# Performance work log

Measured on AMD Instinct MI355X. Metric: run time of the kernel, lower is better.

## Reference

```python
import jax, jax.numpy as jnp
import numpy as np

DIM_HID = 65536
NKERS = 500  # fixed by nn.Linear(dim_hid, 500) in the original module


def setup_inputs() -> dict:
    key = jax.random.key(0)
    k1, k2, k3, k4, k5 = jax.random.split(key, 5)
    inp = jax.random.normal(k1, (DIM_HID,), dtype=jnp.float32)
    weight = jax.random.normal(k2, (NKERS, DIM_HID), dtype=jnp.float32) * (1.0 / np.sqrt(DIM_HID))
    bias = jax.random.normal(k3, (NKERS,), dtype=jnp.float32)
    # variable-width kernels, each kwidths[i] in [1, NKERS]
    kwidths = jax.random.randint(k4, (NKERS,), 1, NKERS + 1, dtype=jnp.int32)
    kernels = jax.random.normal(k5, (NKERS, NKERS), dtype=jnp.float32)
    return {"input": inp, "weight": weight, "bias": bias, "kernels": kernels, "kwidths": kwidths}


def reference(input, weight, bias, kernels, kwidths):
    # y = self.coefs(input): [NKERS]
    y = weight @ input + bias
    # The torch loop  z[:kwidths[i]] += y[i] * kernels[i]  is exactly a
    # weighted sum of zero-padded kernel rows: mask row i beyond kwidths[i].
    col = jnp.arange(NKERS, dtype=kwidths.dtype)
    mask = col[None, :] < kwidths[:, None]            # [NKERS, NKERS] bool
    padded = jnp.where(mask, kernels, 0.0)            # zero-padded kernel bank
    z = y @ padded                                    # [NKERS]
    return z
```

## Files before the change

kernel.cpp:

```cpp
#include <hip/hip_runtime.h>

#define DIM_HID 65536
#define NKERS   500
#define NQ      4
#define QCHUNK  (DIM_HID / NQ)

typedef float f4 __attribute__((ext_vector_type(4)));

__global__ __launch_bounds__(256) void gemv_part_kernel(
    const float* __restrict__ W,
    const float* __restrict__ x,
    float* __restrict__ ws)
{
    const int bid = blockIdx.x;
    const int row = bid >> 2;
    const int q   = bid & 3;
    const int t   = threadIdx.x;

    const f4* __restrict__ Wq =
        reinterpret_cast<const f4*>(W + (size_t)row * DIM_HID + q * QCHUNK);
    const f4* __restrict__ xq =
        reinterpret_cast<const f4*>(x + q * QCHUNK);

    float s = 0.0f;
#pragma unroll 4
    for (int k = 0; k < 16; ++k) {
        const int idx = t + k * 256;
        f4 w = __builtin_nontemporal_load(&Wq[idx]);
        f4 v = xq[idx];
        s = fmaf(w.x, v.x, s);
        s = fmaf(w.y, v.y, s);
        s = fmaf(w.z, v.z, s);
        s = fmaf(w.w, v.w, s);
    }

#pragma unroll
    for (int off = 32; off > 0; off >>= 1)
        s += __shfl_down(s, off, 64);

    __shared__ float wsum[4];
    const int wave = t >> 6;
    const int lane = t & 63;
    if (lane == 0) wsum[wave] = s;
    __syncthreads();

    if (t == 0)
        ws[bid] = (wsum[0] + wsum[1]) + (wsum[2] + wsum[3]);
}

__global__ __launch_bounds__(256) void expand_kernel(
    const float* __restrict__ ws,
    const float* __restrict__ bias,
    const float* __restrict__ kernels,
    const int* __restrict__ kw,
    float* __restrict__ z)
{
    const int j = blockIdx.x;
    const int t = threadIdx.x;
    const f4* __restrict__ wsv = reinterpret_cast<const f4*>(ws);

    float acc = 0.0f;
#pragma unroll
    for (int k = 0; k < 2; ++k) {
        const int i = t + k * 256;
        if (i < NKERS) {
            f4 p = wsv[i];
            const float yi = ((p.x + p.y) + (p.z + p.w)) + bias[i];
            const int   w  = kw[i];
            const float kv = kernels[i * NKERS + j];
            if (j < w) acc = fmaf(yi, kv, acc);
        }
    }

#pragma unroll
    for (int off = 32; off > 0; off >>= 1)
        acc += __shfl_down(acc, off, 64);

    __shared__ float wsum[4];
    const int wave = t >> 6;
    const int lane = t & 63;
    if (lane == 0) wsum[wave] = acc;
    __syncthreads();

    if (t == 0)
        z[j] = (wsum[0] + wsum[1]) + (wsum[2] + wsum[3]);
}

extern "C" void kernel_launch(void* const* d_in, const int* in_sizes, int n_in,
                              void* d_out, int out_size, void* d_ws, size_t ws_size,
                              hipStream_t stream)
{
    const float* input   = (const float*)d_in[0];
    const float* weight  = (const float*)d_in[1];
    const float* bias    = (const float*)d_in[2];
    const float* kernels = (const float*)d_in[3];
    const int*   kwidths = (const int*)d_in[4];
    float* z  = (float*)d_out;
    float* ws = (float*)d_ws;

    gemv_part_kernel<<<NKERS * NQ, 256, 0, stream>>>(weight, input, ws);
    expand_kernel<<<NKERS, 256, 0, stream>>>(ws, bias, kernels, kwidths, z);
}
```

Baseline: 29.76 us.

## Restructure expand stage into row-tiled partial sums plus reduction; drop nontemporal loads

The second stage, which assigned one block per output column and read a strided column of the kernel bank, is replaced by 32 blocks. Each block processes 16 kernel rows with coalesced row reads and writes partial column sums, and a third single-block kernel reduces them. This targets uncoalesced strided access and redundant recomputation of y in every block. It costs an extra kernel launch and a serial reduction over 32 partials. The GEMV weight load also switches from a nontemporal to a normal load.

```diff
diff --git a/kernel.cpp b/kernel.cpp
--- a/kernel.cpp
+++ b/kernel.cpp
@@ -4,6 +4,10 @@
 #define NKERS   500
 #define NQ      4
 #define QCHUNK  (DIM_HID / NQ)
+
+#define ITILE   16
+#define NIB     32
+#define JPAD    512
 
 typedef float f4 __attribute__((ext_vector_type(4)));
 
@@ -26,7 +30,7 @@
 #pragma unroll 4
     for (int k = 0; k < 16; ++k) {
         const int idx = t + k * 256;
-        f4 w = __builtin_nontemporal_load(&Wq[idx]);
+        f4 w = Wq[idx];
         f4 v = xq[idx];
         s = fmaf(w.x, v.x, s);
         s = fmaf(w.y, v.y, s);
@@ -48,42 +52,49 @@
         ws[bid] = (wsum[0] + wsum[1]) + (wsum[2] + wsum[3]);
 }
 
-__global__ __launch_bounds__(256) void expand_kernel(
+__global__ __launch_bounds__(256) void expand_part_kernel(
     const float* __restrict__ ws,
     const float* __restrict__ bias,
     const float* __restrict__ kernels,
     const int* __restrict__ kw,
+    float* __restrict__ partial)
+{
+    const int ib = blockIdx.x;
+    const int t  = threadIdx.x;
+    const int j0 = t;
+    const int j1 = t + 256;
+    const f4* __restrict__ wsv = reinterpret_cast<const f4*>(ws);
+
+    float a0 = 0.0f, a1 = 0.0f;
+#pragma unroll
+    for (int ii = 0; ii < ITILE; ++ii) {
+        const int i = ib * ITILE + ii;
+        if (i < NKERS) {
+            const f4  p  = wsv[i];
+            const float yi = ((p.x + p.y) + (p.z + p.w)) + bias[i];
+            const int   w  = kw[i];
+            const float* krow = kernels + i * NKERS;
+            const float k0 = krow[j0];
+            const float k1 = (j1 < NKERS) ? krow[j1] : 0.0f;
+            if (j0 < w) a0 = fmaf(yi, k0, a0);
+            if (j1 < w) a1 = fmaf(yi, k1, a1);
+        }
+    }
+    partial[ib * JPAD + j0] = a0;
+    partial[ib * JPAD + j1] = a1;
+}
+
+__global__ __launch_bounds__(512) void expand_reduce_kernel(
+    const float* __restrict__ partial,
     float* __restrict__ z)
 {
-    const int j = blockIdx.x;
-    const int t = threadIdx.x;
-    const f4* __restrict__ wsv = reinterpret_cast<const f4*>(ws);
-
-    float acc = 0.0f;
+    const int j = threadIdx.x;
+    if (j >= NKERS) return;
+    float s = 0.0f;
 #pragma unroll
-    for (int k = 0; k < 2; ++k) {
-        const int i = t + k * 256;
-        if (i < NKERS) {
-            f4 p = wsv[i];
-            const float yi = ((p.x + p.y) + (p.z + p.w)) + bias[i];
-            const int   w  = kw[i];
-            const float kv = kernels[i * NKERS + j];
-            if (j < w) acc = fmaf(yi, kv, acc);
-        }
-    }
-
-#pragma unroll
-    for (int off = 32; off > 0; off >>= 1)
-        acc += __shfl_down(acc, off, 64);
-
-    __shared__ float wsum[4];
-    const int wave = t >> 6;
-    const int lane = t & 63;
-    if (lane == 0) wsum[wave] = acc;
-    __syncthreads();
-
-    if (t == 0)
-        z[j] = (wsum[0] + wsum[1]) + (wsum[2] + wsum[3]);
+    for (int ib = 0; ib < NIB; ++ib)
+        s += partial[ib * JPAD + j];
+    z[j] = s;
 }
 
 extern "C" void kernel_launch(void* const* d_in, const int* in_sizes, int n_in,
@@ -97,7 +108,9 @@
     const int*   kwidths = (const int*)d_in[4];
     float* z  = (float*)d_out;
     float* ws = (float*)d_ws;
+    float* pz = ws + 4096;
 
     gemv_part_kernel<<<NKERS * NQ, 256, 0, stream>>>(weight, input, ws);
-    expand_kernel<<<NKERS, 256, 0, stream>>>(ws, bias, kernels, kwidths, z);
+    expand_part_kernel<<<NIB, 256, 0, stream>>>(ws, bias, kernels, kwidths, pz);
+    expand_reduce_kernel<<<1, 512, 0, stream>>>(pz, z);
 }
```

Result: slower. 32.95 us (+10.7%).

## Process four weight rows per GEMV block over sixteen column chunks

Applied to the files above, without the earlier changes.

Each GEMV block now computes partial dot products for four rows over a 4096-element column chunk, so one x load is reused across four weight rows. The grid still has 2000 blocks, and each thread issues four independent wide loads per iteration, which gives more memory parallelism. Sixteen partials per row are written to the workspace and summed in the expand kernel. This adds register pressure and a larger reduction in the second kernel.

```diff
diff --git a/kernel.cpp b/kernel.cpp
--- a/kernel.cpp
+++ b/kernel.cpp
@@ -2,50 +2,70 @@
 
 #define DIM_HID 65536
 #define NKERS   500
-#define NQ      4
-#define QCHUNK  (DIM_HID / NQ)
+#define ROWS_PB 4
+#define NCHUNK  16
+#define CHUNK   (DIM_HID / NCHUNK)
 
 typedef float f4 __attribute__((ext_vector_type(4)));
 
-__global__ __launch_bounds__(256) void gemv_part_kernel(
+__global__ __launch_bounds__(256, 8) void gemv_part_kernel(
     const float* __restrict__ W,
     const float* __restrict__ x,
     float* __restrict__ ws)
 {
     const int bid = blockIdx.x;
-    const int row = bid >> 2;
-    const int q   = bid & 3;
+    const int rg  = bid >> 4;
+    const int q   = bid & 15;
+    const int r0  = rg * ROWS_PB;
     const int t   = threadIdx.x;
 
-    const f4* __restrict__ Wq =
-        reinterpret_cast<const f4*>(W + (size_t)row * DIM_HID + q * QCHUNK);
-    const f4* __restrict__ xq =
-        reinterpret_cast<const f4*>(x + q * QCHUNK);
+    const size_t base = (size_t)r0 * DIM_HID + (size_t)q * CHUNK;
+    const f4* __restrict__ W0 = reinterpret_cast<const f4*>(W + base);
+    const f4* __restrict__ W1 = reinterpret_cast<const f4*>(W + base + DIM_HID);
+    const f4* __restrict__ W2 = reinterpret_cast<const f4*>(W + base + 2 * DIM_HID);
+    const f4* __restrict__ W3 = reinterpret_cast<const f4*>(W + base + 3 * DIM_HID);
+    const f4* __restrict__ xq = reinterpret_cast<const f4*>(x + q * CHUNK);
 
-    float s = 0.0f;
-#pragma unroll 4
-    for (int k = 0; k < 16; ++k) {
+    float s0 = 0.0f, s1 = 0.0f, s2 = 0.0f, s3 = 0.0f;
+#pragma unroll 2
+    for (int k = 0; k < 4; ++k) {
         const int idx = t + k * 256;
-        f4 w = __builtin_nontemporal_load(&Wq[idx]);
-        f4 v = xq[idx];
-        s = fmaf(w.x, v.x, s);
-        s = fmaf(w.y, v.y, s);
-        s = fmaf(w.z, v.z, s);
-        s = fmaf(w.w, v.w, s);
+        const f4 v  = xq[idx];
+        const f4 w0 = __builtin_nontemporal_load(&W0[idx]);
+        const f4 w1 = __builtin_nontemporal_load(&W1[idx]);
+        const f4 w2 = __builtin_nontemporal_load(&W2[idx]);
+        const f4 w3 = __builtin_nontemporal_load(&W3[idx]);
+        s0 = fmaf(w0.x, v.x, s0); s0 = fmaf(w0.y, v.y, s0);
+        s0 = fmaf(w0.z, v.z, s0); s0 = fmaf(w0.w, v.w, s0);
+        s1 = fmaf(w1.x, v.x, s1); s1 = fmaf(w1.y, v.y, s1);
+        s1 = fmaf(w1.z, v.z, s1); s1 = fmaf(w1.w, v.w, s1);
+        s2 = fmaf(w2.x, v.x, s2); s2 = fmaf(w2.y, v.y, s2);
+        s2 = fmaf(w2.z, v.z, s2); s2 = fmaf(w2.w, v.w, s2);
+        s3 = fmaf(w3.x, v.x, s3); s3 = fmaf(w3.y, v.y, s3);
+        s3 = fmaf(w3.z, v.z, s3); s3 = fmaf(w3.w, v.w, s3);
     }
 
 #pragma unroll
-    for (int off = 32; off > 0; off >>= 1)
-        s += __shfl_down(s, off, 64);
+    for (int off = 32; off > 0; off >>= 1) {
+        s0 += __shfl_down(s0, off, 64);
+        s1 += __shfl_down(s1, off, 64);
+        s2 += __shfl_down(s2, off, 64);
+        s3 += __shfl_down(s3, off, 64);
+    }
 
-    __shared__ float wsum[4];
+    __shared__ float wsum[4][4];
     const int wave = t >> 6;
     const int lane = t & 63;
-    if (lane == 0) wsum[wave] = s;
+    if (lane == 0) {
+        wsum[wave][0] = s0; wsum[wave][1] = s1;
+        wsum[wave][2] = s2; wsum[wave][3] = s3;
+    }
     __syncthreads();
 
-    if (t == 0)
-        ws[bid] = (wsum[0] + wsum[1]) + (wsum[2] + wsum[3]);
+    if (t < 4) {
+        float a = wsum[0][t] + wsum[1][t] + wsum[2][t] + wsum[3][t];
+        ws[(size_t)(r0 + t) * NCHUNK + q] = a;
+    }
 }
 
 __global__ __launch_bounds__(256) void expand_kernel(
@@ -64,8 +84,14 @@
     for (int k = 0; k < 2; ++k) {
         const int i = t + k * 256;
         if (i < NKERS) {
-            f4 p = wsv[i];
-            const float yi = ((p.x + p.y) + (p.z + p.w)) + bias[i];
+            const f4 p0 = wsv[i * 4 + 0];
+            const f4 p1 = wsv[i * 4 + 1];
+            const f4 p2 = wsv[i * 4 + 2];
+            const f4 p3 = wsv[i * 4 + 3];
+            const float yi = (((p0.x + p0.y) + (p0.z + p0.w)) +
+                              ((p1.x + p1.y) + (p1.z + p1.w))) +
+                             (((p2.x + p2.y) + (p2.z + p2.w)) +
+                              ((p3.x + p3.y) + (p3.z + p3.w))) + bias[i];
             const int   w  = kw[i];
             const float kv = kernels[i * NKERS + j];
             if (j < w) acc = fmaf(yi, kv, acc);
@@ -98,6 +124,6 @@
     float* z  = (float*)d_out;
     float* ws = (float*)d_ws;
 
-    gemv_part_kernel<<<NKERS * NQ, 256, 0, stream>>>(weight, input, ws);
+    gemv_part_kernel<<<(NKERS / ROWS_PB) * NCHUNK, 256, 0, stream>>>(weight, input, ws);
     expand_kernel<<<NKERS, 256, 0, stream>>>(ws, bias, kernels, kwidths, z);
 }
```

Result: faster. 27.27 us (-8.4%).
